# Kernel optimization log

Measured on AMD Instinct MI355X. Metric: run time of the kernel, lower is better.

Reference implementation:

```python
import jax, jax.numpy as jnp
import numpy as np

BLOCK_SIZE = 64
R_BLOCKS = 64          # r: number of rotation blocks (r * block_size == in_features)
N_ELEMENTS = BLOCK_SIZE * (BLOCK_SIZE - 1) // 2  # 2016
NUM_NEUMANN_TERMS = 5

# strict upper-triangular indices (matches torch.triu_indices(b, b, 1))
_ROWS, _COLS = np.triu_indices(BLOCK_SIZE, 1)


def _cayley_neumann(weight):
    """weight: (r, n_elements) -> batch of orthogonal-ish blocks (r, b, b)."""
    b = BLOCK_SIZE
    M = jnp.zeros((weight.shape[0], b, b), dtype=weight.dtype)
    M = M.at[:, _ROWS, _COLS].set(weight)
    Q = M - jnp.swapaxes(M, -1, -2)           # skew-symmetric (r, b, b)
    I = jnp.eye(b, dtype=weight.dtype)
    # R = I + 2Q + 2Q^2 + ... + 2Q^(terms-1)
    R = I + 2.0 * Q
    Qp = jnp.matmul(Q, Q)
    R = R + 2.0 * Qp
    for _ in range(3, NUM_NEUMANN_TERMS):
        Qp = jnp.matmul(Qp, Q)
        R = R + 2.0 * Qp
    return R


def setup_inputs() -> dict:
    key = jax.random.key(0)
    k_x, k_w = jax.random.split(key)
    x = jax.random.normal(k_x, (8192, 4096), dtype=jnp.float32)
    # small weights so the Neumann series approximates the Cayley transform
    weight = jax.random.normal(k_w, (R_BLOCKS, N_ELEMENTS), dtype=jnp.float32) * 0.01
    return {"x": x, "weight": weight}


def reference(x, weight):
    # x: (N, in_features); block-diagonal rotation applied per 64-wide block
    orth = _cayley_neumann(weight)                      # (r, b, b)
    N = x.shape[0]
    xr = x.reshape(N, R_BLOCKS, BLOCK_SIZE)             # (N, r, b)
    out = jnp.einsum("nrk,rkc->nrc", xr, orth)          # block-diag matmul
    return out.reshape(x.shape)
```

## Files before the change

kernel.cpp:

```cpp
#include <hip/hip_runtime.h>


#define BS 64
#define NW 2016
#define LDP 68


__device__ __forceinline__ void mm_tile_68(const float (*A)[LDP], const float (*Bm)[LDP],
                                           int r0, int c0, float p[4][4]) {
  for (int k = 0; k < 64; k += 4) {
    float4 bv[4], av[4];
#pragma unroll
    for (int u = 0; u < 4; ++u) bv[u] = *(const float4*)&Bm[k + u][c0];
#pragma unroll
    for (int i = 0; i < 4; ++i) av[i] = *(const float4*)&A[r0 + i][k];
#pragma unroll
    for (int u = 0; u < 4; ++u) {
      const float4 b = bv[u];
#pragma unroll
      for (int i = 0; i < 4; ++i) {
        const float a = ((const float*)&av[i])[u];
        p[i][0] += a * b.x;
        p[i][1] += a * b.y;
        p[i][2] += a * b.z;
        p[i][3] += a * b.w;
      }
    }
  }
}

__global__ __launch_bounds__(256) void oft_build_R(const float* __restrict__ w,
                                                   float* __restrict__ Rout) {
  const int r = blockIdx.x;
  const int t = threadIdx.x;
  __shared__ float Q[BS][LDP];
  __shared__ float Pa[BS][LDP];
  __shared__ float Pb[BS][LDP];

  for (int f = t; f < BS * LDP; f += 256) (&Q[0][0])[f] = 0.f;
  __syncthreads();

  for (int i = t; i < NW; i += 256) {
    int row = 0, rem = i;
    while (rem >= 63 - row) { rem -= 63 - row; ++row; }
    const int col = row + 1 + rem;
    const float v = w[r * NW + i];
    Q[row][col] = v;
    Q[col][row] = -v;
  }
  __syncthreads();

  const int tr = t >> 4, tc = t & 15;
  const int r0 = tr * 4, c0 = tc * 4;

  float acc[4][4];
#pragma unroll
  for (int i = 0; i < 4; ++i)
#pragma unroll
    for (int j = 0; j < 4; ++j)
      acc[i][j] = ((r0 + i) == (c0 + j) ? 1.f : 0.f) + 2.f * Q[r0 + i][c0 + j];

  float p[4][4] = {};
  mm_tile_68(Q, Q, r0, c0, p);
#pragma unroll
  for (int i = 0; i < 4; ++i)
#pragma unroll
    for (int j = 0; j < 4; ++j) {
      Pa[r0 + i][c0 + j] = p[i][j];
      acc[i][j] += 2.f * p[i][j];
    }
  __syncthreads();

  float p2[4][4] = {};
  mm_tile_68(Pa, Q, r0, c0, p2);
#pragma unroll
  for (int i = 0; i < 4; ++i)
#pragma unroll
    for (int j = 0; j < 4; ++j) {
      Pb[r0 + i][c0 + j] = p2[i][j];
      acc[i][j] += 2.f * p2[i][j];
    }
  __syncthreads();

  float p3[4][4] = {};
  mm_tile_68(Pb, Q, r0, c0, p3);
#pragma unroll
  for (int i = 0; i < 4; ++i)
#pragma unroll
    for (int j = 0; j < 4; ++j)
      acc[i][j] += 2.f * p3[i][j];

#pragma unroll
  for (int i = 0; i < 4; ++i) {
    float4 v = make_float4(acc[i][0], acc[i][1], acc[i][2], acc[i][3]);
    *(float4*)&Rout[(size_t)r * 4096 + (size_t)(r0 + i) * 64 + c0] = v;
  }
}


__global__ __launch_bounds__(256) void oft_apply(const float* __restrict__ x,
                                                 const float* __restrict__ R,
                                                 float* __restrict__ out) {
  const int r = blockIdx.x;
  const int tile = blockIdx.y;
  const int t = threadIdx.x;

  __shared__ float Rs[BS * BS];
  __shared__ float Xs[BS][LDP];

  const int n0 = tile * 64;

  const float4* Rg = (const float4*)(R + (size_t)r * 4096);
  float4* Rs4 = (float4*)Rs;
#pragma unroll
  for (int i = 0; i < 4; ++i) Rs4[t + 256 * i] = Rg[t + 256 * i];

#pragma unroll
  for (int i = 0; i < 4; ++i) {
    const int f = t + 256 * i;
    const int row = f >> 4;
    const int c4 = (f & 15) << 2;
    *(float4*)&Xs[row][c4] =
        *(const float4*)&x[(size_t)(n0 + row) * 4096 + r * 64 + c4];
  }
  __syncthreads();

  const int tr = t >> 4, tc = t & 15;
  const int c0 = tc * 4, rr0 = tr * 4;

  float acc[4][4] = {};
#pragma unroll 4
  for (int k = 0; k < 64; k += 4) {
    float4 bv[4], av[4];
#pragma unroll
    for (int u = 0; u < 4; ++u) bv[u] = *(const float4*)&Rs[(k + u) * 64 + c0];
#pragma unroll
    for (int i = 0; i < 4; ++i) av[i] = *(const float4*)&Xs[rr0 + i][k];
#pragma unroll
    for (int u = 0; u < 4; ++u) {
      const float4 b = bv[u];
#pragma unroll
      for (int i = 0; i < 4; ++i) {
        const float a = ((const float*)&av[i])[u];
        acc[i][0] += a * b.x;
        acc[i][1] += a * b.y;
        acc[i][2] += a * b.z;
        acc[i][3] += a * b.w;
      }
    }
  }

#pragma unroll
  for (int i = 0; i < 4; ++i) {
    float4 v = make_float4(acc[i][0], acc[i][1], acc[i][2], acc[i][3]);
    *(float4*)&out[(size_t)(n0 + rr0 + i) * 4096 + r * 64 + c0] = v;
  }
}

extern "C" void kernel_launch(void* const* d_in, const int* in_sizes, int n_in,
                              void* d_out, int out_size, void* d_ws, size_t ws_size,
                              hipStream_t stream) {
  const float* x = (const float*)d_in[0];
  const float* w = (const float*)d_in[1];
  float* out = (float*)d_out;
  float* Rws = (float*)d_ws;

  oft_build_R<<<64, 256, 0, stream>>>(w, Rws);
  oft_apply<<<dim3(64, 128), 256, 0, stream>>>(x, Rws, out);
}
```

Measured before the change: 250.7 us.

## Keep rotation column in registers and stream x rows per wave

The apply kernel no longer stages R and x in LDS. Each lane now holds one column of the 64x64 rotation block in registers, and each wave walks 32 rows of x, loading each row uniformly across lanes and doing scalar FMAs. Outputs are written with nontemporal stores, and each block covers 128 rows instead of 64, so the grid is halved. This removes LDS traffic and block-level syncs. The cost is 64 extra VGPRs for R and per-row scalar/broadcast loads of x, which may hurt load efficiency or occupancy.

```diff
diff --git a/kernel.cpp b/kernel.cpp
--- a/kernel.cpp
+++ b/kernel.cpp
@@ -98,62 +98,48 @@
 }
 
 
+#define ROWS_PER_BLOCK 128
+#define ROWS_PER_WAVE 32
+
 __global__ __launch_bounds__(256) void oft_apply(const float* __restrict__ x,
                                                  const float* __restrict__ R,
                                                  float* __restrict__ out) {
   const int r = blockIdx.x;
   const int tile = blockIdx.y;
-  const int t = threadIdx.x;
+  const int lane = threadIdx.x & 63;
+  const int wid = __builtin_amdgcn_readfirstlane((int)(threadIdx.x >> 6));
 
-  __shared__ float Rs[BS * BS];
-  __shared__ float Xs[BS][LDP];
+  float Rcol[64];
+  {
+    const float* Rg = R + (size_t)r * 4096 + lane;
+#pragma unroll
+    for (int k = 0; k < 64; ++k) Rcol[k] = Rg[(size_t)k * 64];
+  }
 
-  const int n0 = tile * 64;
+  const int n0 = tile * ROWS_PER_BLOCK + wid * ROWS_PER_WAVE;
+  const float* __restrict__ xw = x + (size_t)n0 * 4096 + (size_t)r * 64;
+  float* __restrict__ ow = out + (size_t)n0 * 4096 + (size_t)r * 64 + lane;
 
-  const float4* Rg = (const float4*)(R + (size_t)r * 4096);
-  float4* Rs4 = (float4*)Rs;
+  for (int i = 0; i < ROWS_PER_WAVE; i += 2) {
+    const float* __restrict__ xa = xw + (size_t)i * 4096;
+    const float* __restrict__ xb = xa + 4096;
+    float acc0 = 0.f, acc1 = 0.f;
 #pragma unroll
-  for (int i = 0; i < 4; ++i) Rs4[t + 256 * i] = Rg[t + 256 * i];
-
+    for (int c = 0; c < 4; ++c) {
+      float a0[16], a1[16];
 #pragma unroll
-  for (int i = 0; i < 4; ++i) {
-    const int f = t + 256 * i;
-    const int row = f >> 4;
-    const int c4 = (f & 15) << 2;
-    *(float4*)&Xs[row][c4] =
-        *(const float4*)&x[(size_t)(n0 + row) * 4096 + r * 64 + c4];
-  }
-  __syncthreads();
-
-  const int tr = t >> 4, tc = t & 15;
-  const int c0 = tc * 4, rr0 = tr * 4;
-
-  float acc[4][4] = {};
-#pragma unroll 4
-  for (int k = 0; k < 64; k += 4) {
-    float4 bv[4], av[4];
+      for (int k = 0; k < 16; ++k) {
+        a0[k] = xa[c * 16 + k];
+        a1[k] = xb[c * 16 + k];
+      }
 #pragma unroll
-    for (int u = 0; u < 4; ++u) bv[u] = *(const float4*)&Rs[(k + u) * 64 + c0];
-#pragma unroll
-    for (int i = 0; i < 4; ++i) av[i] = *(const float4*)&Xs[rr0 + i][k];
-#pragma unroll
-    for (int u = 0; u < 4; ++u) {
-      const float4 b = bv[u];
-#pragma unroll
-      for (int i = 0; i < 4; ++i) {
-        const float a = ((const float*)&av[i])[u];
-        acc[i][0] += a * b.x;
-        acc[i][1] += a * b.y;
-        acc[i][2] += a * b.z;
-        acc[i][3] += a * b.w;
+      for (int k = 0; k < 16; ++k) {
+        acc0 = fmaf(a0[k], Rcol[c * 16 + k], acc0);
+        acc1 = fmaf(a1[k], Rcol[c * 16 + k], acc1);
       }
     }
-  }
-
-#pragma unroll
-  for (int i = 0; i < 4; ++i) {
-    float4 v = make_float4(acc[i][0], acc[i][1], acc[i][2], acc[i][3]);
-    *(float4*)&out[(size_t)(n0 + rr0 + i) * 4096 + r * 64 + c0] = v;
+    __builtin_nontemporal_store(acc0, ow + (size_t)i * 4096);
+    __builtin_nontemporal_store(acc1, ow + (size_t)(i + 1) * 4096);
   }
 }
 
@@ -166,5 +152,5 @@
   float* Rws = (float*)d_ws;
 
   oft_build_R<<<64, 256, 0, stream>>>(w, Rws);
-  oft_apply<<<dim3(64, 128), 256, 0, stream>>>(x, Rws, out);
+  oft_apply<<<dim3(64, 64), 256, 0, stream>>>(x, Rws, out);
 }
```

New measurement: 406.4 us. +62.1%, slower.

## Restructure block-diagonal apply with per-wave 8x8 register tiles and swizzled transposed LDS

Applied to the files above, without the earlier changes.

The apply kernel now gives each wave its own 64-row slab of x, so a block covers 256 rows and the grid shrinks fourfold. Each x tile is stored transposed in LDS with an XOR swizzle so reads are vectorised and avoid bank conflicts. Each thread accumulates an 8x8 output tile instead of 4x4, which raises FMA work per LDS load. Output uses nontemporal stores to limit cache pollution. In exchange, LDS use per block rises to about 80KB and register pressure goes up, which can reduce occupancy.

```diff
diff --git a/kernel.cpp b/kernel.cpp
--- a/kernel.cpp
+++ b/kernel.cpp
@@ -4,6 +4,8 @@
 #define BS 64
 #define NW 2016
 #define LDP 68
+
+typedef float vf4 __attribute__((ext_vector_type(4)));
 
 
 __device__ __forceinline__ void mm_tile_68(const float (*A)[LDP], const float (*Bm)[LDP],
@@ -104,56 +106,91 @@
   const int r = blockIdx.x;
   const int tile = blockIdx.y;
   const int t = threadIdx.x;
-
-  __shared__ float Rs[BS * BS];
-  __shared__ float Xs[BS][LDP];
-
-  const int n0 = tile * 64;
-
-  const float4* Rg = (const float4*)(R + (size_t)r * 4096);
-  float4* Rs4 = (float4*)Rs;
-#pragma unroll
-  for (int i = 0; i < 4; ++i) Rs4[t + 256 * i] = Rg[t + 256 * i];
-
-#pragma unroll
-  for (int i = 0; i < 4; ++i) {
-    const int f = t + 256 * i;
-    const int row = f >> 4;
-    const int c4 = (f & 15) << 2;
-    *(float4*)&Xs[row][c4] =
-        *(const float4*)&x[(size_t)(n0 + row) * 4096 + r * 64 + c4];
-  }
-  __syncthreads();
-
-  const int tr = t >> 4, tc = t & 15;
-  const int c0 = tc * 4, rr0 = tr * 4;
-
-  float acc[4][4] = {};
-#pragma unroll 4
-  for (int k = 0; k < 64; k += 4) {
-    float4 bv[4], av[4];
-#pragma unroll
-    for (int u = 0; u < 4; ++u) bv[u] = *(const float4*)&Rs[(k + u) * 64 + c0];
-#pragma unroll
-    for (int i = 0; i < 4; ++i) av[i] = *(const float4*)&Xs[rr0 + i][k];
+  const int lane = t & 63;
+  const int wv = t >> 6;
+
+  __shared__ float Rs[64 * 64];
+  __shared__ float Xt[4][64 * 64];
+
+  const int n0 = tile * 256 + wv * 64;
+
+  {
+    const float4* Rg = (const float4*)(R + (size_t)r * 4096);
+    float4* Rs4 = (float4*)Rs;
+#pragma unroll
+    for (int i = 0; i < 4; ++i) Rs4[t + 256 * i] = Rg[t + 256 * i];
+  }
+
+  float* __restrict__ Xw = &Xt[wv][0];
+  {
+    const int rq = lane >> 2;
+    const int kq0 = lane & 3;
+    const float* xg = x + (size_t)n0 * 4096 + (size_t)r * 64;
+#pragma unroll
+    for (int i = 0; i < 4; ++i) {
+      const int kq = kq0 + 4 * i;
+      const float4 v0 = *(const float4*)&xg[(size_t)(rq * 4 + 0) * 4096 + kq * 4];
+      const float4 v1 = *(const float4*)&xg[(size_t)(rq * 4 + 1) * 4096 + kq * 4];
+      const float4 v2 = *(const float4*)&xg[(size_t)(rq * 4 + 2) * 4096 + kq * 4];
+      const float4 v3 = *(const float4*)&xg[(size_t)(rq * 4 + 3) * 4096 + kq * 4];
+      const float4 w0 = make_float4(v0.x, v1.x, v2.x, v3.x);
+      const float4 w1 = make_float4(v0.y, v1.y, v2.y, v3.y);
+      const float4 w2 = make_float4(v0.z, v1.z, v2.z, v3.z);
+      const float4 w3 = make_float4(v0.w, v1.w, v2.w, v3.w);
+#pragma unroll
+      for (int c = 0; c < 4; ++c) {
+        const int k = kq * 4 + c;
+        const int slot = rq ^ (k & 7);
+        const float4 wc = (c == 0) ? w0 : (c == 1) ? w1 : (c == 2) ? w2 : w3;
+        *(float4*)&Xw[k * 64 + slot * 4] = wc;
+      }
+    }
+  }
+  __syncthreads();
+
+  const int tr = lane >> 3;
+  const int tc = lane & 7;
+
+  float acc[8][8];
+#pragma unroll
+  for (int i = 0; i < 8; ++i)
+#pragma unroll
+    for (int j = 0; j < 8; ++j) acc[i][j] = 0.f;
+
+  for (int k0 = 0; k0 < 64; k0 += 4) {
+    float4 a[4][2], b[4][2];
 #pragma unroll
     for (int u = 0; u < 4; ++u) {
-      const float4 b = bv[u];
-#pragma unroll
-      for (int i = 0; i < 4; ++i) {
-        const float a = ((const float*)&av[i])[u];
-        acc[i][0] += a * b.x;
-        acc[i][1] += a * b.y;
-        acc[i][2] += a * b.z;
-        acc[i][3] += a * b.w;
-      }
-    }
-  }
-
-#pragma unroll
-  for (int i = 0; i < 4; ++i) {
-    float4 v = make_float4(acc[i][0], acc[i][1], acc[i][2], acc[i][3]);
-    *(float4*)&out[(size_t)(n0 + rr0 + i) * 4096 + r * 64 + c0] = v;
+      const int k = k0 + u;
+      const int s0 = ((2 * tr + 0) ^ (k & 7)) * 4;
+      const int s1 = ((2 * tr + 1) ^ (k & 7)) * 4;
+      a[u][0] = *(const float4*)&Xw[k * 64 + s0];
+      a[u][1] = *(const float4*)&Xw[k * 64 + s1];
+      b[u][0] = *(const float4*)&Rs[k * 64 + tc * 8];
+      b[u][1] = *(const float4*)&Rs[k * 64 + tc * 8 + 4];
+    }
+#pragma unroll
+    for (int u = 0; u < 4; ++u) {
+      const float av[8] = {a[u][0].x, a[u][0].y, a[u][0].z, a[u][0].w,
+                           a[u][1].x, a[u][1].y, a[u][1].z, a[u][1].w};
+      const float bv[8] = {b[u][0].x, b[u][0].y, b[u][0].z, b[u][0].w,
+                           b[u][1].x, b[u][1].y, b[u][1].z, b[u][1].w};
+#pragma unroll
+      for (int i = 0; i < 8; ++i)
+#pragma unroll
+        for (int j = 0; j < 8; ++j)
+          acc[i][j] = fmaf(av[i], bv[j], acc[i][j]);
+    }
+  }
+
+  float* __restrict__ og = out + (size_t)(n0 + tr * 8) * 4096 + (size_t)r * 64 + tc * 8;
+#pragma unroll
+  for (int i = 0; i < 8; ++i) {
+    vf4 lo, hi;
+    lo.x = acc[i][0]; lo.y = acc[i][1]; lo.z = acc[i][2]; lo.w = acc[i][3];
+    hi.x = acc[i][4]; hi.y = acc[i][5]; hi.z = acc[i][6]; hi.w = acc[i][7];
+    __builtin_nontemporal_store(lo, (vf4*)&og[(size_t)i * 4096]);
+    __builtin_nontemporal_store(hi, (vf4*)&og[(size_t)i * 4096 + 4]);
   }
 }
 
@@ -166,5 +203,5 @@
   float* Rws = (float*)d_ws;
 
   oft_build_R<<<64, 256, 0, stream>>>(w, Rws);
-  oft_apply<<<dim3(64, 128), 256, 0, stream>>>(x, Rws, out);
-}
+  oft_apply<<<dim3(64, 32), 256, 0, stream>>>(x, Rws, out);
+}
```

New measurement: 272.6 us. +8.7%, slower.
